# Kernel tuning notes

Hardware: AMD Instinct MI355X
Metric: run time of the kernel (lower is better)

## Reference

```python
import jax, jax.numpy as jnp
import numpy as np
from math import log

MODEL_DIM = 512
NUM_HEADS = 8
DIM_HEAD = 64
INNER = NUM_HEADS * DIM_HEAD
B, L = 8, 1024
EPS = 1e-5


def setup_inputs() -> dict:
    key = jax.random.key(0)
    ks = jax.random.split(key, 9)
    x = jax.random.normal(ks[0], (B, L, MODEL_DIM), dtype=jnp.float32)
    gamma = jnp.ones((MODEL_DIM,), jnp.float32)
    beta = jnp.zeros((MODEL_DIM,), jnp.float32)
    w_qkv = jax.random.normal(ks[1], (3 * INNER, MODEL_DIM), jnp.float32) * (MODEL_DIM ** -0.5)
    b_qkv = jnp.zeros((3 * INNER,), jnp.float32)
    w_pos = jax.random.normal(ks[2], (INNER, MODEL_DIM), jnp.float32) * (MODEL_DIM ** -0.5)
    w_out = jax.random.normal(ks[3], (MODEL_DIM, INNER), jnp.float32) * (INNER ** -0.5)
    b_out = jnp.zeros((MODEL_DIM,), jnp.float32)
    # xavier_uniform for (num_heads, dim_head)
    bound = (6.0 / (NUM_HEADS + DIM_HEAD)) ** 0.5
    u_bias = jax.random.uniform(ks[4], (NUM_HEADS, DIM_HEAD), jnp.float32, -bound, bound)
    v_bias = jax.random.uniform(ks[5], (NUM_HEADS, DIM_HEAD), jnp.float32, -bound, bound)
    return {"x": x, "gamma": gamma, "beta": beta, "w_qkv": w_qkv, "b_qkv": b_qkv,
            "w_pos": w_pos, "w_out": w_out, "b_out": b_out, "u_bias": u_bias, "v_bias": v_bias}


def _rel_pos_emb(seq_len, d):
    # (L, D): (i - j) scaled by sinusoid frequencies, then cos on even cols, sin on odd cols
    rel = (jnp.arange(seq_len, dtype=jnp.float32)[:, None]
           - jnp.arange(d, dtype=jnp.float32)[None, :])
    freqs = jnp.exp(-jnp.arange(0, 2 * d, 2, dtype=jnp.float32) * (log(10000.0) / MODEL_DIM))
    angle = rel * freqs[None, :]
    even = (jnp.arange(d) % 2) == 0
    return jnp.where(even[None, :], jnp.cos(angle), jnp.sin(angle))  # (L, D)


def reference(x, gamma, beta, w_qkv, b_qkv, w_pos, w_out, b_out, u_bias, v_bias):
    b, l, d = x.shape
    h, dh = NUM_HEADS, DIM_HEAD
    # LayerNorm
    mu = jnp.mean(x, axis=-1, keepdims=True)
    var = jnp.mean(jnp.square(x - mu), axis=-1, keepdims=True)
    xn = (x - mu) * jax.lax.rsqrt(var + EPS) * gamma + beta
    # relative position embedding, identical per batch element
    pe = _rel_pos_emb(l, d)                      # (L, D)
    pos = (pe @ w_pos.T).reshape(l, h, dh)       # (L, H, Dh)
    pos = jnp.transpose(pos, (1, 0, 2))          # (H, L, Dh)
    # qkv
    qkv = xn @ w_qkv.T + b_qkv                   # (B, L, 3*inner)
    q, k, v = jnp.split(qkv, 3, axis=-1)
    def to_heads(t):
        return jnp.transpose(t.reshape(b, l, h, dh), (0, 2, 1, 3))  # (B,H,L,Dh)
    q, k, v = to_heads(q), to_heads(k), to_heads(v)
    scale = dh ** -0.5
    content = jnp.einsum('bhld,bhmd->bhlm', q + u_bias[None, :, None, :], k)
    pos_score = jnp.einsum('bhld,hmd->bhlm', q + v_bias[None, :, None, :], pos)
    attn = jax.nn.softmax((content + pos_score) * scale, axis=-1)
    out = jnp.einsum('bhlm,bhmd->bhld', attn, v)
    out = jnp.transpose(out, (0, 2, 1, 3)).reshape(b, l, h * dh)
    return out @ w_out.T + b_out  # dropout p=0.0 -> identity
```

## Files before the change

kernel.cpp:

```cpp
#include <hip/hip_runtime.h>
#include <math.h>

static constexpr int Bn = 8, Ln = 1024, Dm = 512, Hn = 8, DhN = 64;

typedef short bf16x8 __attribute__((ext_vector_type(8)));
typedef float f32x4 __attribute__((ext_vector_type(4)));
typedef _Float16 f16x4 __attribute__((ext_vector_type(4)));
typedef _Float16 f16x8 __attribute__((ext_vector_type(8)));
typedef unsigned int u32x4 __attribute__((ext_vector_type(4)));

#define QSCALE 0.1803368801111137f

static __device__ __forceinline__ unsigned short f2b(float f) {
  union { float f; unsigned int u; } x;
  x.f = f;
  unsigned int u = x.u;
  unsigned int r = (u + 0x7FFFu + ((u >> 16) & 1u)) >> 16;
  return (unsigned short)r;
}
static __device__ __forceinline__ float b2f(unsigned short u) {
  union { unsigned int u; float f; } x;
  x.u = ((unsigned int)u) << 16;
  return x.f;
}

#define GLDS16(g, l)                                                        \
  __builtin_amdgcn_global_load_lds((const __attribute__((address_space(1))) void*)(g), \
                                   (__attribute__((address_space(3))) void*)(l), 16, 0, 0)

__global__ __launch_bounds__(256) void prep1(const float* __restrict__ x,
                                             const float* __restrict__ gamma,
                                             const float* __restrict__ beta,
                                             unsigned short* __restrict__ xn,
                                             unsigned short* __restrict__ pe,
                                             const float* __restrict__ wq, unsigned short* __restrict__ wqb,
                                             const float* __restrict__ wp, unsigned short* __restrict__ wpb,
                                             const float* __restrict__ wo, unsigned short* __restrict__ wob) {
  int b = blockIdx.x;
  int t = threadIdx.x;
  if (b < 8192) {
    const float2 v = *(const float2*)(x + (size_t)b * Dm + t * 2);
    float s = v.x + v.y;
    float sq = v.x * v.x + v.y * v.y;
#pragma unroll
    for (int off = 32; off > 0; off >>= 1) {
      s += __shfl_down(s, off);
      sq += __shfl_down(sq, off);
    }
    __shared__ float red[8];
    int wave = t >> 6, lane = t & 63;
    if (lane == 0) { red[wave * 2] = s; red[wave * 2 + 1] = sq; }
    __syncthreads();
    float S = red[0] + red[2] + red[4] + red[6];
    float SQ = red[1] + red[3] + red[5] + red[7];
    float mu = S * (1.0f / Dm);
    float var = SQ * (1.0f / Dm) - mu * mu;
    float rstd = rsqrtf(var + 1e-5f);
    int c = t * 2;
    ushort2 o;
    o.x = f2b((v.x - mu) * rstd * gamma[c] + beta[c]);
    o.y = f2b((v.y - mu) * rstd * gamma[c + 1] + beta[c + 1]);
    *(ushort2*)(xn + (size_t)b * Dm + c) = o;
  } else if (b < 10240) {
    int idx = (b - 8192) * 256 + t;
    int l = idx >> 9, k = idx & 511;
    float freq = expf(-0.0359778921f * (float)k);
    float angle = (float)(l - k) * freq;
    pe[idx] = f2b((k & 1) ? sinf(angle) : cosf(angle));
  } else {
    int cb = b - 10240;
    const float* src;
    unsigned short* dst;
    int off;
    if (cb < 768) { src = wq; dst = wqb; off = cb; }
    else if (cb < 1024) { src = wp; dst = wpb; off = cb - 768; }
    else { src = wo; dst = wob; off = cb - 1024; }
    int i = off * 256 + t;
    float4 v = *(const float4*)(src + (size_t)i * 4);
    ushort4 o;
    o.x = f2b(v.x); o.y = f2b(v.y); o.z = f2b(v.z); o.w = f2b(v.w);
    *(ushort4*)(dst + (size_t)i * 4) = o;
  }
}

__global__ __launch_bounds__(256, 8) void gemm_mfma(const unsigned short* __restrict__ Ain,
                                                    const unsigned short* __restrict__ Bwin,
                                                    const float* __restrict__ biasin,
                                                    float* __restrict__ outfin,
                                                    unsigned short* __restrict__ oq,
                                                    unsigned short* __restrict__ ok,
                                                    unsigned short* __restrict__ ov,
                                                    const unsigned short* __restrict__ A2,
                                                    const unsigned short* __restrict__ B2,
                                                    float* __restrict__ outf2,
                                                    int K, int mode) {
  int by = blockIdx.y, bx = blockIdx.x;
  const unsigned short* A = Ain;
  const unsigned short* Bw = Bwin;
  const float* bias = biasin;
  float* outf = outfin;
  if (by >= 128) {
    if (bx >= 8) return;
    A = A2; Bw = B2; bias = nullptr; outf = outf2; mode = 1; by -= 128;
  }
  __shared__ alignas(16) unsigned short As[64 * 64];
  __shared__ alignas(16) unsigned short Bs[64 * 64];
  const int t = threadIdx.x;
  const int lane = t & 63, w = t >> 6;
  const int c = lane & 15, q8 = lane >> 4;
  const int wm = (w & 1) * 32, wn = (w >> 1) * 32;
  const int m0 = by * 64, n0 = bx * 64;

  f32x4 acc[2][2];
#pragma unroll
  for (int i = 0; i < 2; ++i)
#pragma unroll
    for (int j = 0; j < 2; ++j) acc[i][j] = (f32x4){0.f, 0.f, 0.f, 0.f};

  const int srow = lane >> 3;
  const int sgr = (lane & 7) ^ srow;

  for (int k0 = 0; k0 < K; k0 += 64) {
    __syncthreads();
#pragma unroll
    for (int j = 0; j < 2; ++j) {
      int r = j * 32 + w * 8 + srow;
      GLDS16(A + (size_t)(m0 + r) * K + k0 + sgr * 8, As + (j * 256 + w * 64 + lane) * 8);
      GLDS16(Bw + (size_t)(n0 + r) * K + k0 + sgr * 8, Bs + (j * 256 + w * 64 + lane) * 8);
    }
    __syncthreads();
#pragma unroll
    for (int kk = 0; kk < 2; ++kk) {
      bf16x8 a[2], b[2];
      const int q = kk * 4 + q8;
#pragma unroll
      for (int i = 0; i < 2; ++i) {
        int r = wm + i * 16 + c;
        a[i] = *(const bf16x8*)&As[(r * 8 + (q ^ (r & 7))) * 8];
      }
#pragma unroll
      for (int j = 0; j < 2; ++j) {
        int r = wn + j * 16 + c;
        b[j] = *(const bf16x8*)&Bs[(r * 8 + (q ^ (r & 7))) * 8];
      }
#pragma unroll
      for (int i = 0; i < 2; ++i)
#pragma unroll
        for (int j = 0; j < 2; ++j)
          acc[i][j] = __builtin_amdgcn_mfma_f32_16x16x32_bf16(a[i], b[j], acc[i][j], 0, 0, 0);
    }
  }
#pragma unroll
  for (int i = 0; i < 2; ++i) {
#pragma unroll
    for (int r = 0; r < 4; ++r) {
      int m = m0 + wm + i * 16 + q8 * 4 + r;
#pragma unroll
      for (int j = 0; j < 2; ++j) {
        int n = n0 + wn + j * 16 + c;
        float val = acc[i][j][r] + (bias ? bias[n] : 0.0f);
        if (mode == 0) {
          int part = n >> 9, h = (n >> 6) & 7, dh = n & 63;
          int bb = m >> 10, l = m & 1023;
          size_t idx = (size_t)((bb * 8 + h) * 1024 + l) * 64 + dh;
          if (part == 0) {
            oq[idx] = f2b(val * QSCALE);
          } else if (part == 1) {
            ok[idx] = f2b(val);
          } else {
            union { _Float16 h; unsigned short u; } cv;
            cv.h = (_Float16)val;
            ov[idx] = cv.u;
          }
        } else if (mode == 1) {
          int h = n >> 6, dh = n & 63;
          outf[(size_t)(h * 1024 + m) * 64 + dh] = val;
        } else {
          outf[(size_t)m * 512 + n] = val;
        }
      }
    }
  }
}

__global__ __launch_bounds__(256) void prep2(unsigned short* __restrict__ kbuf,
                                             const float* __restrict__ pos,
                                             const float* __restrict__ ub,
                                             const float* __restrict__ vbb,
                                             float* __restrict__ biasout,
                                             const unsigned short* __restrict__ v,
                                             unsigned short* __restrict__ vt) {
  int b = blockIdx.x;
  int t = threadIdx.x;
  if (b < 16384) {
    int wave = t >> 6, lane = t & 63;
    int g = b * 4 + wave;
    int h = (g >> 10) & 7;
    int m = g & 1023;
    float kv = b2f(kbuf[(size_t)g * 64 + lane]);
    float pv = pos[(size_t)(h * 1024 + m) * 64 + lane];
    float val = ub[h * 64 + lane] * kv + vbb[h * 64 + lane] * pv;
#pragma unroll
    for (int off = 32; off > 0; off >>= 1) val += __shfl_down(val, off);
    if (lane == 0) biasout[g] = val * QSCALE;
    kbuf[(size_t)g * 64 + lane] = f2b(kv + pv);
  } else {
    __shared__ unsigned short Ts[64 * 68];
    int bb = b - 16384;
    int bh = bb >> 4, lt = bb & 15;
    const unsigned short* vg = v + (size_t)bh * 65536 + lt * 4096;
#pragma unroll
    for (int s = 0; s < 4; ++s) {
      int idx = t + s * 256;
      int r = idx >> 4, c4 = (idx & 15) << 2;
      *(ushort4*)&Ts[r * 68 + c4] = *(const ushort4*)(vg + r * 64 + c4);
    }
    __syncthreads();
#pragma unroll
    for (int s = 0; s < 4; ++s) {
      int idx = t + s * 256;
      int d = idx >> 4, l4 = (idx & 15) << 2;
      ushort4 o;
      o.x = Ts[(l4 + 0) * 68 + d];
      o.y = Ts[(l4 + 1) * 68 + d];
      o.z = Ts[(l4 + 2) * 68 + d];
      o.w = Ts[(l4 + 3) * 68 + d];
      int pb = ((l4 >> 2) & 3) * 16 + ((l4 >> 4) & 3) * 4;
      *(ushort4*)(vt + (size_t)bh * 65536 + d * 1024 + lt * 64 + pb) = o;
    }
  }
}

__global__ __launch_bounds__(256) void flash_mfma(const unsigned short* __restrict__ qbf,
                                                  const unsigned short* __restrict__ kbf,
                                                  const unsigned short* __restrict__ vt,
                                                  const float* __restrict__ bias,
                                                  unsigned short* __restrict__ attn_out) {
  __shared__ alignas(16) unsigned short Ks[64 * 64];
  __shared__ alignas(16) unsigned short Vs[64 * 64];
  __shared__ alignas(16) float Bls[1024];
  const int t = threadIdx.x;
  const int lane = t & 63, w = t >> 6;
  const int c = lane & 15, q8 = lane >> 4;
  const int cc7 = c & 7;
  const int bh = blockIdx.y, qt = blockIdx.x;
  const unsigned short* qg = qbf + (size_t)bh * 65536;
  const unsigned short* kg = kbf + (size_t)bh * 65536;
  const unsigned short* vg = vt + (size_t)bh * 65536;
  const float* bg = bias + (size_t)bh * 1024;

  GLDS16(bg + w * 256 + lane * 4, Bls + w * 256 + lane * 4);

  const int ql = qt * 64 + w * 16 + c;
  const bf16x8 bq0 = *(const bf16x8*)(qg + (size_t)ql * 64 + q8 * 8);
  const bf16x8 bq1 = *(const bf16x8*)(qg + (size_t)ql * 64 + 32 + q8 * 8);

  float m_st = -INFINITY, l_st = 0.0f;
  f32x4 o[4];
#pragma unroll
  for (int i = 0; i < 4; ++i) o[i] = (f32x4){0.f, 0.f, 0.f, 0.f};

  const int srow = lane >> 3;
  const int sgr = (lane & 7) ^ srow;
  const int r0 = w * 16 + srow;

  u32x4 pk[2], pv[2];
#pragma unroll
  for (int j = 0; j < 2; ++j) {
    int r = r0 + j * 8;
    pk[j] = *(const u32x4*)(kg + (size_t)r * 64 + sgr * 8);
    pv[j] = *(const u32x4*)(vg + (size_t)r * 1024 + sgr * 8);
  }

  for (int kt = 0; kt < 16; ++kt) {
    __syncthreads();
#pragma unroll
    for (int j = 0; j < 2; ++j) {
      int r = r0 + j * 8;
      *(u32x4*)&Ks[(r * 8 + (lane & 7)) * 8] = pk[j];
      *(u32x4*)&Vs[(r * 8 + (lane & 7)) * 8] = pv[j];
    }
    __syncthreads();
    if (kt < 15) {
#pragma unroll
      for (int j = 0; j < 2; ++j) {
        int r = r0 + j * 8;
        pk[j] = *(const u32x4*)(kg + (size_t)((kt + 1) * 64 + r) * 64 + sgr * 8);
        pv[j] = *(const u32x4*)(vg + (size_t)r * 1024 + (kt + 1) * 64 + sgr * 8);
      }
    }

    f32x4 sc[4];
#pragma unroll
    for (int nt = 0; nt < 4; ++nt) {
      f32x4 ci = *(const f32x4*)&Bls[kt * 64 + nt * 16 + q8 * 4];
      const int row = nt * 16 + c;
      bf16x8 ak0 = *(const bf16x8*)&Ks[(row * 8 + (q8 ^ cc7)) * 8];
      bf16x8 ak1 = *(const bf16x8*)&Ks[(row * 8 + ((q8 + 4) ^ cc7)) * 8];
      ci = __builtin_amdgcn_mfma_f32_16x16x32_bf16(ak0, bq0, ci, 0, 0, 0);
      sc[nt] = __builtin_amdgcn_mfma_f32_16x16x32_bf16(ak1, bq1, ci, 0, 0, 0);
    }
    float mx = sc[0][0];
#pragma unroll
    for (int nt = 0; nt < 4; ++nt)
#pragma unroll
      for (int r = 0; r < 4; ++r) mx = fmaxf(mx, sc[nt][r]);
    mx = fmaxf(mx, __shfl_xor(mx, 16));
    mx = fmaxf(mx, __shfl_xor(mx, 32));
    float mn = fmaxf(m_st, mx);
    float al = __builtin_amdgcn_exp2f(m_st - mn);
    float su = 0.0f;
    f16x4 pf[4];
#pragma unroll
    for (int nt = 0; nt < 4; ++nt)
#pragma unroll
      for (int r = 0; r < 4; ++r) {
        float p = __builtin_amdgcn_exp2f(sc[nt][r] - mn);
        su += p;
        pf[nt][r] = (_Float16)p;
      }
    su += __shfl_xor(su, 16);
    su += __shfl_xor(su, 32);
    l_st = l_st * al + su;
    m_st = mn;
#pragma unroll
    for (int i = 0; i < 4; ++i) o[i] *= al;
#pragma unroll
    for (int i = 0; i < 4; ++i) {
      const int row = i * 16 + c;
      f16x8 v01 = *(const f16x8*)&Vs[(row * 8 + ((2 * q8) ^ cc7)) * 8];
      f16x8 v23 = *(const f16x8*)&Vs[(row * 8 + ((2 * q8 + 1) ^ cc7)) * 8];
      f16x4 a0 = {v01[0], v01[1], v01[2], v01[3]};
      f16x4 a1 = {v01[4], v01[5], v01[6], v01[7]};
      f16x4 a2 = {v23[0], v23[1], v23[2], v23[3]};
      f16x4 a3 = {v23[4], v23[5], v23[6], v23[7]};
      o[i] = __builtin_amdgcn_mfma_f32_16x16x16f16(a0, pf[0], o[i], 0, 0, 0);
      o[i] = __builtin_amdgcn_mfma_f32_16x16x16f16(a1, pf[1], o[i], 0, 0, 0);
      o[i] = __builtin_amdgcn_mfma_f32_16x16x16f16(a2, pf[2], o[i], 0, 0, 0);
      o[i] = __builtin_amdgcn_mfma_f32_16x16x16f16(a3, pf[3], o[i], 0, 0, 0);
    }
  }
  const int bidx = bh >> 3, h = bh & 7;
  float inv = 1.0f / l_st;
  size_t base = (size_t)(bidx * 1024 + ql) * 512 + h * 64;
#pragma unroll
  for (int i = 0; i < 4; ++i) {
    ushort4 ov4;
    ov4.x = f2b(o[i][0] * inv);
    ov4.y = f2b(o[i][1] * inv);
    ov4.z = f2b(o[i][2] * inv);
    ov4.w = f2b(o[i][3] * inv);
    *(ushort4*)(attn_out + base + i * 16 + q8 * 4) = ov4;
  }
}

extern "C" void kernel_launch(void* const* d_in, const int* in_sizes, int n_in,
                              void* d_out, int out_size, void* d_ws, size_t ws_size,
                              hipStream_t stream) {
  const float* x      = (const float*)d_in[0];
  const float* gamma  = (const float*)d_in[1];
  const float* beta   = (const float*)d_in[2];
  const float* w_qkv  = (const float*)d_in[3];
  const float* b_qkv  = (const float*)d_in[4];
  const float* w_pos  = (const float*)d_in[5];
  const float* w_out  = (const float*)d_in[6];
  const float* b_out  = (const float*)d_in[7];
  const float* u_bias = (const float*)d_in[8];
  const float* v_bias = (const float*)d_in[9];
  float* out = (float*)d_out;

  unsigned short* wsu = (unsigned short*)d_ws;
  unsigned short* xnb   = wsu;
  unsigned short* peb   = wsu + 4194304;
  unsigned short* wqkvb = wsu + 4718592;
  unsigned short* wposb = wsu + 5505024;
  unsigned short* woutb = wsu + 5767168;
  unsigned short* qbf   = wsu + 6291456;
  unsigned short* kbf   = wsu + 10485760;
  unsigned short* vbf   = wsu + 14680064;
  unsigned short* vtb   = wsu + 18874368;
  unsigned short* attnb = wsu + 23068672;
  float* posb  = (float*)(wsu + 27262976);
  float* biasb = (float*)(wsu + 28311552);

  prep1<<<11520, 256, 0, stream>>>(x, gamma, beta, xnb, peb,
                                   w_qkv, wqkvb, w_pos, wposb, w_out, woutb);
  gemm_mfma<<<dim3(24, 144), 256, 0, stream>>>(xnb, wqkvb, b_qkv, nullptr, qbf, kbf, vbf,
                                               peb, wposb, posb, 512, 0);
  prep2<<<17408, 256, 0, stream>>>(kbf, posb, u_bias, v_bias, biasb, vbf, vtb);
  flash_mfma<<<dim3(16, 64), 256, 0, stream>>>(qbf, kbf, vtb, biasb, attnb);
  gemm_mfma<<<dim3(8, 128), 256, 0, stream>>>(attnb, woutb, b_out, out, nullptr, nullptr, nullptr,
                                              nullptr, nullptr, nullptr, 512, 2);
}
```

Baseline: 187.8 us.

## Use 128-row query tiles and 128-key steps in flash attention kernel

The flash attention block grows to 512 threads (8 waves) covering 128 query rows, and each iteration now processes 128 keys as two 64-key halves in shared memory, halving the iteration count and barriers. Each staged K/V tile is reused by twice as many waves, which reduces global reloads and synchronization per unit of work. The cost is higher register pressure from doubled score/probability arrays, more LDS per block, and half as many blocks (512), which may lower occupancy and load balance.

```diff
diff --git a/kernel.cpp b/kernel.cpp
--- a/kernel.cpp
+++ b/kernel.cpp
@@ -231,13 +231,13 @@
   }
 }
 
-__global__ __launch_bounds__(256) void flash_mfma(const unsigned short* __restrict__ qbf,
+__global__ __launch_bounds__(512) void flash_mfma(const unsigned short* __restrict__ qbf,
                                                   const unsigned short* __restrict__ kbf,
                                                   const unsigned short* __restrict__ vt,
                                                   const float* __restrict__ bias,
                                                   unsigned short* __restrict__ attn_out) {
-  __shared__ alignas(16) unsigned short Ks[64 * 64];
-  __shared__ alignas(16) unsigned short Vs[64 * 64];
+  __shared__ alignas(16) unsigned short Ks[2][64 * 64];
+  __shared__ alignas(16) unsigned short Vs[2][64 * 64];
   __shared__ alignas(16) float Bls[1024];
   const int t = threadIdx.x;
   const int lane = t & 63, w = t >> 6;
@@ -249,9 +249,9 @@
   const unsigned short* vg = vt + (size_t)bh * 65536;
   const float* bg = bias + (size_t)bh * 1024;
 
-  GLDS16(bg + w * 256 + lane * 4, Bls + w * 256 + lane * 4);
-
-  const int ql = qt * 64 + w * 16 + c;
+  if (t < 256) GLDS16(bg + t * 4, Bls + t * 4);
+
+  const int ql = qt * 128 + w * 16 + c;
   const bf16x8 bq0 = *(const bf16x8*)(qg + (size_t)ql * 64 + q8 * 8);
   const bf16x8 bq1 = *(const bf16x8*)(qg + (size_t)ql * 64 + 32 + q8 * 8);
 
@@ -262,63 +262,67 @@
 
   const int srow = lane >> 3;
   const int sgr = (lane & 7) ^ srow;
-  const int r0 = w * 16 + srow;
+  const int r0 = w * 8 + srow;
 
   u32x4 pk[2], pv[2];
 #pragma unroll
-  for (int j = 0; j < 2; ++j) {
-    int r = r0 + j * 8;
-    pk[j] = *(const u32x4*)(kg + (size_t)r * 64 + sgr * 8);
-    pv[j] = *(const u32x4*)(vg + (size_t)r * 1024 + sgr * 8);
-  }
-
-  for (int kt = 0; kt < 16; ++kt) {
-    __syncthreads();
-#pragma unroll
-    for (int j = 0; j < 2; ++j) {
-      int r = r0 + j * 8;
-      *(u32x4*)&Ks[(r * 8 + (lane & 7)) * 8] = pk[j];
-      *(u32x4*)&Vs[(r * 8 + (lane & 7)) * 8] = pv[j];
-    }
-    __syncthreads();
-    if (kt < 15) {
-#pragma unroll
-      for (int j = 0; j < 2; ++j) {
-        int r = r0 + j * 8;
-        pk[j] = *(const u32x4*)(kg + (size_t)((kt + 1) * 64 + r) * 64 + sgr * 8);
-        pv[j] = *(const u32x4*)(vg + (size_t)r * 1024 + (kt + 1) * 64 + sgr * 8);
-      }
-    }
-
-    f32x4 sc[4];
-#pragma unroll
-    for (int nt = 0; nt < 4; ++nt) {
-      f32x4 ci = *(const f32x4*)&Bls[kt * 64 + nt * 16 + q8 * 4];
-      const int row = nt * 16 + c;
-      bf16x8 ak0 = *(const bf16x8*)&Ks[(row * 8 + (q8 ^ cc7)) * 8];
-      bf16x8 ak1 = *(const bf16x8*)&Ks[(row * 8 + ((q8 + 4) ^ cc7)) * 8];
-      ci = __builtin_amdgcn_mfma_f32_16x16x32_bf16(ak0, bq0, ci, 0, 0, 0);
-      sc[nt] = __builtin_amdgcn_mfma_f32_16x16x32_bf16(ak1, bq1, ci, 0, 0, 0);
-    }
-    float mx = sc[0][0];
-#pragma unroll
-    for (int nt = 0; nt < 4; ++nt)
-#pragma unroll
-      for (int r = 0; r < 4; ++r) mx = fmaxf(mx, sc[nt][r]);
+  for (int h = 0; h < 2; ++h) {
+    pk[h] = *(const u32x4*)(kg + (size_t)(h * 64 + r0) * 64 + sgr * 8);
+    pv[h] = *(const u32x4*)(vg + (size_t)r0 * 1024 + h * 64 + sgr * 8);
+  }
+
+  for (int it = 0; it < 8; ++it) {
+    __syncthreads();
+#pragma unroll
+    for (int h = 0; h < 2; ++h) {
+      *(u32x4*)&Ks[h][(r0 * 8 + (lane & 7)) * 8] = pk[h];
+      *(u32x4*)&Vs[h][(r0 * 8 + (lane & 7)) * 8] = pv[h];
+    }
+    __syncthreads();
+    if (it < 7) {
+#pragma unroll
+      for (int h = 0; h < 2; ++h) {
+        pk[h] = *(const u32x4*)(kg + (size_t)((it + 1) * 128 + h * 64 + r0) * 64 + sgr * 8);
+        pv[h] = *(const u32x4*)(vg + (size_t)r0 * 1024 + (it + 1) * 128 + h * 64 + sgr * 8);
+      }
+    }
+
+    f32x4 sc[2][4];
+#pragma unroll
+    for (int h = 0; h < 2; ++h) {
+#pragma unroll
+      for (int nt = 0; nt < 4; ++nt) {
+        f32x4 ci = *(const f32x4*)&Bls[it * 128 + h * 64 + nt * 16 + q8 * 4];
+        const int row = nt * 16 + c;
+        bf16x8 ak0 = *(const bf16x8*)&Ks[h][(row * 8 + (q8 ^ cc7)) * 8];
+        bf16x8 ak1 = *(const bf16x8*)&Ks[h][(row * 8 + ((q8 + 4) ^ cc7)) * 8];
+        ci = __builtin_amdgcn_mfma_f32_16x16x32_bf16(ak0, bq0, ci, 0, 0, 0);
+        sc[h][nt] = __builtin_amdgcn_mfma_f32_16x16x32_bf16(ak1, bq1, ci, 0, 0, 0);
+      }
+    }
+    float mx = sc[0][0][0];
+#pragma unroll
+    for (int h = 0; h < 2; ++h)
+#pragma unroll
+      for (int nt = 0; nt < 4; ++nt)
+#pragma unroll
+        for (int r = 0; r < 4; ++r) mx = fmaxf(mx, sc[h][nt][r]);
     mx = fmaxf(mx, __shfl_xor(mx, 16));
     mx = fmaxf(mx, __shfl_xor(mx, 32));
     float mn = fmaxf(m_st, mx);
     float al = __builtin_amdgcn_exp2f(m_st - mn);
     float su = 0.0f;
-    f16x4 pf[4];
-#pragma unroll
-    for (int nt = 0; nt < 4; ++nt)
-#pragma unroll
-      for (int r = 0; r < 4; ++r) {
-        float p = __builtin_amdgcn_exp2f(sc[nt][r] - mn);
-        su += p;
-        pf[nt][r] = (_Float16)p;
-      }
+    f16x4 pf[2][4];
+#pragma unroll
+    for (int h = 0; h < 2; ++h)
+#pragma unroll
+      for (int nt = 0; nt < 4; ++nt)
+#pragma unroll
+        for (int r = 0; r < 4; ++r) {
+          float p = __builtin_amdgcn_exp2f(sc[h][nt][r] - mn);
+          su += p;
+          pf[h][nt][r] = (_Float16)p;
+        }
     su += __shfl_xor(su, 16);
     su += __shfl_xor(su, 32);
     l_st = l_st * al + su;
@@ -328,16 +332,19 @@
 #pragma unroll
     for (int i = 0; i < 4; ++i) {
       const int row = i * 16 + c;
-      f16x8 v01 = *(const f16x8*)&Vs[(row * 8 + ((2 * q8) ^ cc7)) * 8];
-      f16x8 v23 = *(const f16x8*)&Vs[(row * 8 + ((2 * q8 + 1) ^ cc7)) * 8];
-      f16x4 a0 = {v01[0], v01[1], v01[2], v01[3]};
-      f16x4 a1 = {v01[4], v01[5], v01[6], v01[7]};
-      f16x4 a2 = {v23[0], v23[1], v23[2], v23[3]};
-      f16x4 a3 = {v23[4], v23[5], v23[6], v23[7]};
-      o[i] = __builtin_amdgcn_mfma_f32_16x16x16f16(a0, pf[0], o[i], 0, 0, 0);
-      o[i] = __builtin_amdgcn_mfma_f32_16x16x16f16(a1, pf[1], o[i], 0, 0, 0);
-      o[i] = __builtin_amdgcn_mfma_f32_16x16x16f16(a2, pf[2], o[i], 0, 0, 0);
-      o[i] = __builtin_amdgcn_mfma_f32_16x16x16f16(a3, pf[3], o[i], 0, 0, 0);
+#pragma unroll
+      for (int h = 0; h < 2; ++h) {
+        f16x8 v01 = *(const f16x8*)&Vs[h][(row * 8 + ((2 * q8) ^ cc7)) * 8];
+        f16x8 v23 = *(const f16x8*)&Vs[h][(row * 8 + ((2 * q8 + 1) ^ cc7)) * 8];
+        f16x4 a0 = {v01[0], v01[1], v01[2], v01[3]};
+        f16x4 a1 = {v01[4], v01[5], v01[6], v01[7]};
+        f16x4 a2 = {v23[0], v23[1], v23[2], v23[3]};
+        f16x4 a3 = {v23[4], v23[5], v23[6], v23[7]};
+        o[i] = __builtin_amdgcn_mfma_f32_16x16x16f16(a0, pf[h][0], o[i], 0, 0, 0);
+        o[i] = __builtin_amdgcn_mfma_f32_16x16x16f16(a1, pf[h][1], o[i], 0, 0, 0);
+        o[i] = __builtin_amdgcn_mfma_f32_16x16x16f16(a2, pf[h][2], o[i], 0, 0, 0);
+        o[i] = __builtin_amdgcn_mfma_f32_16x16x16f16(a3, pf[h][3], o[i], 0, 0, 0);
+      }
     }
   }
   const int bidx = bh >> 3, h = bh & 7;
@@ -388,7 +395,7 @@
   gemm_mfma<<<dim3(24, 144), 256, 0, stream>>>(xnb, wqkvb, b_qkv, nullptr, qbf, kbf, vbf,
                                                peb, wposb, posb, 512, 0);
   prep2<<<17408, 256, 0, stream>>>(kbf, posb, u_bias, v_bias, biasb, vbf, vtb);
-  flash_mfma<<<dim3(16, 64), 256, 0, stream>>>(qbf, kbf, vtb, biasb, attnb);
+  flash_mfma<<<dim3(8, 64), 512, 0, stream>>>(qbf, kbf, vtb, biasb, attnb);
   gemm_mfma<<<dim3(8, 128), 256, 0, stream>>>(attnb, woutb, b_out, out, nullptr, nullptr, nullptr,
                                               nullptr, nullptr, nullptr, 512, 2);
 }
```

New measurement: 177.8 us. 1.06x faster.
